# Optimization experiments

Hardware: AMD Instinct MI355X
Metric: run time of the kernel (lower is better)

Reference implementation:

```python
import jax, jax.numpy as jnp
import numpy as np

NUM_HEADS = 6
ATTN_TH = 0.0
NEG_INF = -10000.0  # masked-score fill for threshold pruning


def setup_inputs() -> dict:
    key = jax.random.key(0)
    k1, k2, k3 = jax.random.split(key, 3)
    B, N, C = 8, 1024, 384
    x = jax.random.normal(k1, (B, N, C), dtype=jnp.float32)
    # Linear weights (torch layout: [out, in]), scaled like default init
    w_qkv = jax.random.normal(k2, (3 * C, C), dtype=jnp.float32) * (1.0 / np.sqrt(C))
    b_qkv = jnp.zeros((3 * C,), dtype=jnp.float32)
    w_proj = jax.random.normal(k3, (C, C), dtype=jnp.float32) * (1.0 / np.sqrt(C))
    b_proj = jnp.zeros((C,), dtype=jnp.float32)
    return {"x": x, "w_qkv": w_qkv, "b_qkv": b_qkv, "w_proj": w_proj, "b_proj": b_proj}


def reference(x, w_qkv, b_qkv, w_proj, b_proj):
    B, N, C = x.shape
    H = NUM_HEADS
    D = C // H
    scale = D ** -0.5
    # QAct nodes are identity (quant=False); QLinear is a plain linear.
    qkv = jnp.einsum('bnc,oc->bno', x, w_qkv) + b_qkv          # [B,N,3C]
    qkv = qkv.reshape(B, N, 3, H, D).transpose(2, 0, 3, 1, 4)   # [3,B,H,N,D]
    q, k, v = qkv[0], qkv[1], qkv[2]
    attn = jnp.einsum('bhnd,bhmd->bhnm', q, k) * scale          # [B,H,N,N]
    # Threshold pruning: scores below Attn_Th are masked out of the softmax.
    attn = jnp.where(attn < ATTN_TH, NEG_INF, attn)
    attn = jax.nn.softmax(attn, axis=-1)
    out = jnp.einsum('bhnm,bhmd->bhnd', attn, v)                # [B,H,N,D]
    out = out.transpose(0, 2, 1, 3).reshape(B, N, C)
    out = jnp.einsum('bnc,oc->bno', out, w_proj) + b_proj
    return out
```

## Files before the change

### kernel.cpp

```cpp
#include <hip/hip_runtime.h>
#include <hip/hip_bf16.h>


typedef __attribute__((__ext_vector_type__(8))) __bf16 bf16x8;
typedef __attribute__((__ext_vector_type__(8))) unsigned short ushort8;
typedef __attribute__((__ext_vector_type__(4))) unsigned short ushort4v;
typedef __attribute__((__ext_vector_type__(4))) short short4v;
typedef __attribute__((__ext_vector_type__(4))) float f32x4;

#define NX 3145728
#define NQ 442368

__device__ __forceinline__ f32x4 mfma32(bf16x8 a, bf16x8 b, f32x4 c) {
    return __builtin_amdgcn_mfma_f32_16x16x32_bf16(a, b, c, 0, 0, 0);
}
__device__ __forceinline__ f32x4 mfma16(short4v a, short4v b, f32x4 c) {
    return __builtin_amdgcn_mfma_f32_16x16x16bf16_1k(a, b, c, 0, 0, 0);
}

__device__ __forceinline__ unsigned short f2bf(float f) {
    union { float f; unsigned int i; } x; x.f = f;
    unsigned int u = x.i;
    return (unsigned short)((u + 0x7fffu + ((u >> 16) & 1u)) >> 16);
}

__device__ __forceinline__ void dma16(const unsigned short* g, unsigned short* l) {
    __builtin_amdgcn_global_load_lds(
        (const __attribute__((address_space(1))) unsigned int*)g,
        (__attribute__((address_space(3))) unsigned int*)l, 16, 0, 0);
}

__global__ __launch_bounds__(256) void cvt_bf16(
    const float* __restrict__ x, const float* __restrict__ wq, const float* __restrict__ wp,
    unsigned short* __restrict__ xb, unsigned short* __restrict__ wqb, unsigned short* __restrict__ wpb)
{
    int i = blockIdx.x * 256 + threadIdx.x;
    const float* src; unsigned short* dst; int off;
    if (i < NX / 4)              { src = x;  dst = xb;  off = i * 4; }
    else if (i < (NX + NQ) / 4)  { src = wq; dst = wqb; off = i * 4 - NX; }
    else                         { src = wp; dst = wpb; off = i * 4 - NX - NQ; }
    float4 v = *(const float4*)(src + off);
    ushort4v r;
    r[0] = f2bf(v.x); r[1] = f2bf(v.y); r[2] = f2bf(v.z); r[3] = f2bf(v.w);
    *(ushort4v*)(dst + off) = r;
}

template <int MODE, int TM>
__global__ __launch_bounds__(TM * 2) void gemm_bt(
    const unsigned short* __restrict__ A,
    const unsigned short* __restrict__ B,
    const float* __restrict__ bias,
    unsigned short* __restrict__ qg,
    unsigned short* __restrict__ kg,
    unsigned short* __restrict__ vg,
    float* __restrict__ out,
    int M, int N, int K)
{
    const int tid  = threadIdx.x;
    const int lane = tid & 63;
    const int wave = tid >> 6;
    const int l15  = lane & 15;
    const int quad = lane >> 4;
    const int m0 = blockIdx.x * TM;
    const int n0 = blockIdx.y * 128;
    const int wm = (wave >> 1) * 64;
    const int wn = (wave & 1) * 64;

    __shared__ __align__(16) unsigned short As[2 * TM * 32];
    __shared__ __align__(16) unsigned short Bs[2 * 128 * 32];

    f32x4 acc[4][4];
    #pragma unroll
    for (int i = 0; i < 4; ++i)
        #pragma unroll
        for (int j = 0; j < 4; ++j)
            acc[i][j] = (f32x4){0.f, 0.f, 0.f, 0.f};

    auto stage = [&](int k0, int buf) {
        #pragma unroll
        for (int t = 0; t < 2; ++t) {
            int i = tid + t * TM * 2;
            dma16(A + (size_t)(m0 + (i >> 2)) * K + k0 + (i & 3) * 8,
                  As + buf * TM * 32 + t * TM * 16 + wave * 512);
        }
        #pragma unroll
        for (int t = 0; t < 512 / (TM * 2); ++t) {
            int i = tid + t * TM * 2;
            dma16(B + (size_t)(n0 + (i >> 2)) * K + k0 + (i & 3) * 8,
                  Bs + buf * 4096 + t * TM * 16 + wave * 512);
        }
    };

    const int nk = K >> 5;
    stage(0, 0);
    for (int ki = 0; ki < nk; ++ki) {
        __syncthreads();
        if (ki + 1 < nk) stage((ki + 1) << 5, (ki + 1) & 1);
        const unsigned short* as = As + (ki & 1) * TM * 32;
        const unsigned short* bs = Bs + (ki & 1) * 4096;

        bf16x8 af[4], bff[4];
        #pragma unroll
        for (int mt = 0; mt < 4; ++mt)
            af[mt] = *(const bf16x8*)(as + (wm + mt * 16 + l15) * 32 + quad * 8);
        #pragma unroll
        for (int nt = 0; nt < 4; ++nt)
            bff[nt] = *(const bf16x8*)(bs + (wn + nt * 16 + l15) * 32 + quad * 8);
        #pragma unroll
        for (int mt = 0; mt < 4; ++mt)
            #pragma unroll
            for (int nt = 0; nt < 4; ++nt)
                acc[mt][nt] = mfma32(af[mt], bff[nt], acc[mt][nt]);
    }

    if constexpr (MODE == 0) {
        if (n0 < 384) {
            #pragma unroll
            for (int nt = 0; nt < 4; ++nt) {
                int n = n0 + wn + nt * 16 + l15;
                float bv = bias[n];
                #pragma unroll
                for (int mt = 0; mt < 4; ++mt) {
                    int mbase = m0 + wm + mt * 16 + quad * 4;
                    #pragma unroll
                    for (int r = 0; r < 4; ++r)
                        qg[(size_t)(mbase + r) * 384 + n] = f2bf((acc[mt][nt][r] + bv) * 0.125f);
                }
            }
        } else if (n0 < 768) {
            #pragma unroll
            for (int nt = 0; nt < 4; ++nt) {
                int n = n0 + wn + nt * 16 + l15;
                float bv = bias[n];
                int c2 = n - 384;
                int h = c2 >> 6, ck = c2 & 63;
                int half = ck >> 5, qd = (ck >> 3) & 3, j = ck & 7;
                #pragma unroll
                for (int mt = 0; mt < 4; ++mt) {
                    int mbase = m0 + wm + mt * 16 + quad * 4;
                    #pragma unroll
                    for (int r = 0; r < 4; ++r) {
                        int tok = mbase + r;
                        int b = tok >> 10, kv = tok & 1023;
                        int kt = kv >> 4, lk = kv & 15;
                        kg[(size_t)(b * 6 + h) * 65536 +
                           ((((size_t)kt * 2 + half) * 4 + qd) * 16 + lk) * 8 + j]
                            = f2bf(acc[mt][nt][r] + bv);
                    }
                }
            }
        } else {
            #pragma unroll
            for (int nt = 0; nt < 4; ++nt) {
                int n = n0 + wn + nt * 16 + l15;
                float bv = bias[n];
                int c2 = n - 768;
                int h = c2 >> 6, d = c2 & 63;
                int dt = d >> 4, lv = d & 15;
                #pragma unroll
                for (int mt = 0; mt < 4; ++mt) {
                    int mbase = m0 + wm + mt * 16 + quad * 4;
                    int b = mbase >> 10, kvb = mbase & 1023;
                    int cc = kvb >> 6, jt = (kvb >> 4) & 3, qd = (kvb >> 2) & 3;
                    ushort4v pk;
                    #pragma unroll
                    for (int r = 0; r < 4; ++r) pk[r] = f2bf(acc[mt][nt][r] + bv);
                    *(ushort4v*)(vg + (size_t)(b * 6 + h) * 65536 + (size_t)cc * 4096 +
                                 ((((jt * 2 + (dt >> 1)) * 4 + qd) * 16 + lv) * 2 + (dt & 1)) * 4)
                        = pk;
                }
            }
        }
    } else {
        #pragma unroll
        for (int nt = 0; nt < 4; ++nt) {
            int n = n0 + wn + nt * 16 + l15;
            float bv = bias[n];
            #pragma unroll
            for (int mt = 0; mt < 4; ++mt) {
                int mbase = m0 + wm + mt * 16 + quad * 4;
                #pragma unroll
                for (int r = 0; r < 4; ++r)
                    out[(size_t)(mbase + r) * N + n] = acc[mt][nt][r] + bv;
            }
        }
    }
}

__global__ __launch_bounds__(256) void attn_fused(
    const unsigned short* __restrict__ qg,
    const unsigned short* __restrict__ kg,
    const unsigned short* __restrict__ vg,
    unsigned short* __restrict__ aout)
{
    const int tid  = threadIdx.x;
    const int wave = tid >> 6;
    const int lane = tid & 63;
    const int l15  = lane & 15;
    const int quad = lane >> 4;
    const int id = blockIdx.x;
    const int s  = id % 48;
    const int qt = id / 48;
    const int b  = s / 6;
    const int h  = s % 6;

    const size_t rowbase = (size_t)b * 1024;
    const unsigned short* Kslab = kg + (size_t)s * 65536;
    const unsigned short* Vslab = vg + (size_t)s * 65536;
    const int q0 = qt * 64 + wave * 16;

    __shared__ __align__(16) unsigned short Kb[2 * 4096];
    __shared__ __align__(16) unsigned short Vb[2 * 4096];

    bf16x8 aq0, aq1;
    {
        const unsigned short* qrow = qg + (rowbase + q0 + l15) * 384 + h * 64 + quad * 8;
        aq0 = *(const bf16x8*)qrow;
        aq1 = *(const bf16x8*)(qrow + 32);
    }

    f32x4 accO[4];
    #pragma unroll
    for (int dt = 0; dt < 4; ++dt) accO[dt] = (f32x4){0.f, 0.f, 0.f, 0.f};
    float lsum = 0.f;

    auto stage = [&](int c, int buf) {
        #pragma unroll
        for (int t = 0; t < 2; ++t) {
            int i = tid + t * 256;
            dma16(Kslab + (size_t)c * 4096 + i * 8, Kb + buf * 4096 + t * 2048 + wave * 512);
            dma16(Vslab + (size_t)c * 4096 + i * 8, Vb + buf * 4096 + t * 2048 + wave * 512);
        }
    };

    stage(0, 0);
    for (int c = 0; c < 16; ++c) {
        __syncthreads();
        if (c + 1 < 16) stage(c + 1, (c + 1) & 1);
        const unsigned short* kb = Kb + (c & 1) * 4096;
        const unsigned short* vb = Vb + (c & 1) * 4096;

        #pragma unroll
        for (int kt = 0; kt < 4; ++kt) {
            bf16x8 ka  = *(const bf16x8*)(kb + (((kt * 2 + 0) * 4 + quad) * 16 + l15) * 8);
            bf16x8 kbf = *(const bf16x8*)(kb + (((kt * 2 + 1) * 4 + quad) * 16 + l15) * 8);
            f32x4 z = (f32x4){0.f, 0.f, 0.f, 0.f};
            z = mfma32(ka, aq0, z);
            z = mfma32(kbf, aq1, z);

            float e[4];
            #pragma unroll
            for (int r = 0; r < 4; ++r) {
                float sc = z[r];
                sc = (sc < 0.f) ? 0.f : __expf(sc);
                lsum += sc;
                e[r] = sc;
            }
            union { __hip_bfloat162 h2[2]; short4v v; } pu;
            pu.h2[0] = __float22bfloat162_rn(float2{e[0], e[1]});
            pu.h2[1] = __float22bfloat162_rn(float2{e[2], e[3]});
            short4v p = pu.v;

            #pragma unroll
            for (int dtp = 0; dtp < 2; ++dtp) {
                union { bf16x8 w; short4v s4[2]; } vv;
                vv.w = *(const bf16x8*)(vb + (((kt * 2 + dtp) * 4 + quad) * 16 + l15) * 8);
                accO[dtp * 2 + 0] = mfma16(vv.s4[0], p, accO[dtp * 2 + 0]);
                accO[dtp * 2 + 1] = mfma16(vv.s4[1], p, accO[dtp * 2 + 1]);
            }
        }
    }

    lsum += __shfl_xor(lsum, 16, 64);
    lsum += __shfl_xor(lsum, 32, 64);
    float inv = 1.0f / lsum;

    unsigned short* orow = aout + (rowbase + q0 + l15) * 384 + h * 64 + quad * 4;
    #pragma unroll
    for (int dt = 0; dt < 4; ++dt) {
        ushort4v pk;
        #pragma unroll
        for (int r = 0; r < 4; ++r) pk[r] = f2bf(accO[dt][r] * inv);
        *(ushort4v*)(orow + dt * 16) = pk;
    }
}

extern "C" void kernel_launch(void* const* d_in, const int* in_sizes, int n_in,
                              void* d_out, int out_size, void* d_ws, size_t ws_size,
                              hipStream_t stream) {
    const float* x      = (const float*)d_in[0];
    const float* w_qkv  = (const float*)d_in[1];
    const float* b_qkv  = (const float*)d_in[2];
    const float* w_proj = (const float*)d_in[3];
    const float* b_proj = (const float*)d_in[4];
    float* out = (float*)d_out;

    unsigned short* qg   = (unsigned short*)d_ws;
    unsigned short* kgp  = qg   + (size_t)NX;
    unsigned short* vgp  = kgp  + (size_t)NX;
    unsigned short* aout = vgp  + (size_t)NX;
    unsigned short* xb   = aout + (size_t)NX;
    unsigned short* wqb  = xb   + (size_t)NX;
    unsigned short* wpb  = wqb  + (size_t)NQ;

    cvt_bf16<<<3648, 256, 0, stream>>>(x, w_qkv, w_proj, xb, wqb, wpb);
    gemm_bt<0, 256><<<dim3(32, 9), 512, 0, stream>>>(
        xb, wqb, b_qkv, qg, kgp, vgp, nullptr, 8192, 1152, 384);
    attn_fused<<<768, 256, 0, stream>>>(qg, kgp, vgp, aout);
    gemm_bt<1, 128><<<dim3(64, 3), 256, 0, stream>>>(
        aout, wpb, b_proj, nullptr, nullptr, nullptr, out, 8192, 384, 384);
}
```

Before: 129.5 us.

## Process two query tiles per wave and read K/V directly from global memory

Each wave now handles 32 query rows in two 16-row tiles, so every K and V fragment it loads feeds twice as many MFMAs. The LDS double-buffered staging and the per-chunk __syncthreads are removed, and K/V fragments are loaded straight from global memory, relying on cache for reuse across waves. The grid is halved to 384 blocks. This raises register pressure, halves the number of blocks in flight, and leaves the global loads without explicit prefetching or latency hiding.

```diff
diff --git a/kernel.cpp b/kernel.cpp
--- a/kernel.cpp
+++ b/kernel.cpp
@@ -207,81 +207,87 @@
     const size_t rowbase = (size_t)b * 1024;
     const unsigned short* Kslab = kg + (size_t)s * 65536;
     const unsigned short* Vslab = vg + (size_t)s * 65536;
-    const int q0 = qt * 64 + wave * 16;
-
-    __shared__ __align__(16) unsigned short Kb[2 * 4096];
-    __shared__ __align__(16) unsigned short Vb[2 * 4096];
-
-    bf16x8 aq0, aq1;
+    const int q0 = qt * 128 + wave * 32;
+
+    bf16x8 aqA0, aqA1, aqB0, aqB1;
     {
-        const unsigned short* qrow = qg + (rowbase + q0 + l15) * 384 + h * 64 + quad * 8;
-        aq0 = *(const bf16x8*)qrow;
-        aq1 = *(const bf16x8*)(qrow + 32);
-    }
-
-    f32x4 accO[4];
+        const unsigned short* qrowA = qg + (rowbase + q0 + l15) * 384 + h * 64 + quad * 8;
+        const unsigned short* qrowB = qrowA + (size_t)16 * 384;
+        aqA0 = *(const bf16x8*)qrowA;
+        aqA1 = *(const bf16x8*)(qrowA + 32);
+        aqB0 = *(const bf16x8*)qrowB;
+        aqB1 = *(const bf16x8*)(qrowB + 32);
+    }
+
+    f32x4 accA[4], accB[4];
     #pragma unroll
-    for (int dt = 0; dt < 4; ++dt) accO[dt] = (f32x4){0.f, 0.f, 0.f, 0.f};
-    float lsum = 0.f;
-
-    auto stage = [&](int c, int buf) {
-        #pragma unroll
-        for (int t = 0; t < 2; ++t) {
-            int i = tid + t * 256;
-            dma16(Kslab + (size_t)c * 4096 + i * 8, Kb + buf * 4096 + t * 2048 + wave * 512);
-            dma16(Vslab + (size_t)c * 4096 + i * 8, Vb + buf * 4096 + t * 2048 + wave * 512);
-        }
-    };
-
-    stage(0, 0);
+    for (int dt = 0; dt < 4; ++dt) {
+        accA[dt] = (f32x4){0.f, 0.f, 0.f, 0.f};
+        accB[dt] = (f32x4){0.f, 0.f, 0.f, 0.f};
+    }
+    float lsumA = 0.f, lsumB = 0.f;
+
     for (int c = 0; c < 16; ++c) {
-        __syncthreads();
-        if (c + 1 < 16) stage(c + 1, (c + 1) & 1);
-        const unsigned short* kb = Kb + (c & 1) * 4096;
-        const unsigned short* vb = Vb + (c & 1) * 4096;
+        const unsigned short* kb = Kslab + (size_t)c * 4096;
+        const unsigned short* vb = Vslab + (size_t)c * 4096;
 
         #pragma unroll
         for (int kt = 0; kt < 4; ++kt) {
             bf16x8 ka  = *(const bf16x8*)(kb + (((kt * 2 + 0) * 4 + quad) * 16 + l15) * 8);
             bf16x8 kbf = *(const bf16x8*)(kb + (((kt * 2 + 1) * 4 + quad) * 16 + l15) * 8);
-            f32x4 z = (f32x4){0.f, 0.f, 0.f, 0.f};
-            z = mfma32(ka, aq0, z);
-            z = mfma32(kbf, aq1, z);
-
-            float e[4];
+
+            f32x4 zA = (f32x4){0.f, 0.f, 0.f, 0.f};
+            f32x4 zB = (f32x4){0.f, 0.f, 0.f, 0.f};
+            zA = mfma32(ka, aqA0, zA);  zA = mfma32(kbf, aqA1, zA);
+            zB = mfma32(ka, aqB0, zB);  zB = mfma32(kbf, aqB1, zB);
+
+            float eA[4], eB[4];
             #pragma unroll
             for (int r = 0; r < 4; ++r) {
-                float sc = z[r];
-                sc = (sc < 0.f) ? 0.f : __expf(sc);
-                lsum += sc;
-                e[r] = sc;
-            }
-            union { __hip_bfloat162 h2[2]; short4v v; } pu;
-            pu.h2[0] = __float22bfloat162_rn(float2{e[0], e[1]});
-            pu.h2[1] = __float22bfloat162_rn(float2{e[2], e[3]});
-            short4v p = pu.v;
+                float sa = zA[r];
+                sa = (sa < 0.f) ? 0.f : __expf(sa);
+                lsumA += sa; eA[r] = sa;
+                float sb = zB[r];
+                sb = (sb < 0.f) ? 0.f : __expf(sb);
+                lsumB += sb; eB[r] = sb;
+            }
+            union { __hip_bfloat162 h2[2]; short4v v; } pA, pB;
+            pA.h2[0] = __float22bfloat162_rn(float2{eA[0], eA[1]});
+            pA.h2[1] = __float22bfloat162_rn(float2{eA[2], eA[3]});
+            pB.h2[0] = __float22bfloat162_rn(float2{eB[0], eB[1]});
+            pB.h2[1] = __float22bfloat162_rn(float2{eB[2], eB[3]});
 
             #pragma unroll
             for (int dtp = 0; dtp < 2; ++dtp) {
                 union { bf16x8 w; short4v s4[2]; } vv;
                 vv.w = *(const bf16x8*)(vb + (((kt * 2 + dtp) * 4 + quad) * 16 + l15) * 8);
-                accO[dtp * 2 + 0] = mfma16(vv.s4[0], p, accO[dtp * 2 + 0]);
-                accO[dtp * 2 + 1] = mfma16(vv.s4[1], p, accO[dtp * 2 + 1]);
-            }
-        }
-    }
-
-    lsum += __shfl_xor(lsum, 16, 64);
-    lsum += __shfl_xor(lsum, 32, 64);
-    float inv = 1.0f / lsum;
-
-    unsigned short* orow = aout + (rowbase + q0 + l15) * 384 + h * 64 + quad * 4;
+                accA[dtp * 2 + 0] = mfma16(vv.s4[0], pA.v, accA[dtp * 2 + 0]);
+                accA[dtp * 2 + 1] = mfma16(vv.s4[1], pA.v, accA[dtp * 2 + 1]);
+                accB[dtp * 2 + 0] = mfma16(vv.s4[0], pB.v, accB[dtp * 2 + 0]);
+                accB[dtp * 2 + 1] = mfma16(vv.s4[1], pB.v, accB[dtp * 2 + 1]);
+            }
+        }
+    }
+
+    lsumA += __shfl_xor(lsumA, 16, 64);
+    lsumA += __shfl_xor(lsumA, 32, 64);
+    lsumB += __shfl_xor(lsumB, 16, 64);
+    lsumB += __shfl_xor(lsumB, 32, 64);
+    float invA = 1.0f / lsumA;
+    float invB = 1.0f / lsumB;
+
+    unsigned short* orowA = aout + (rowbase + q0 + l15) * 384 + h * 64 + quad * 4;
+    unsigned short* orowB = orowA + (size_t)16 * 384;
     #pragma unroll
     for (int dt = 0; dt < 4; ++dt) {
-        ushort4v pk;
-        #pragma unroll
-        for (int r = 0; r < 4; ++r) pk[r] = f2bf(accO[dt][r] * inv);
-        *(ushort4v*)(orow + dt * 16) = pk;
+        ushort4v pkA, pkB;
+        #pragma unroll
+        for (int r = 0; r < 4; ++r) {
+            pkA[r] = f2bf(accA[dt][r] * invA);
+            pkB[r] = f2bf(accB[dt][r] * invB);
+        }
+        *(ushort4v*)(orowA + dt * 16) = pkA;
+        *(ushort4v*)(orowB + dt * 16) = pkB;
     }
 }
 
@@ -306,7 +312,7 @@
     cvt_bf16<<<3648, 256, 0, stream>>>(x, w_qkv, w_proj, xb, wqb, wpb);
     gemm_bt<0, 256><<<dim3(32, 9), 512, 0, stream>>>(
         xb, wqb, b_qkv, qg, kgp, vgp, nullptr, 8192, 1152, 384);
-    attn_fused<<<768, 256, 0, stream>>>(qg, kgp, vgp, aout);
+    attn_fused<<<384, 256, 0, stream>>>(qg, kgp, vgp, aout);
     gemm_bt<1, 128><<<dim3(64, 3), 256, 0, stream>>>(
         aout, wpb, b_proj, nullptr, nullptr, nullptr, out, 8192, 384, 384);
 }
```

New measurement: 142.4 us. +10.0%, slower.
